# Performance work log

Hardware: AMD Instinct MI355X
Metric: run time of the kernel (lower is better)

## Reference

```python
import jax, jax.numpy as jnp
from jax import lax
import numpy as np

HEADS, SAMPLES = 4, 8
B, C, D, H, W = 1, 64, 16, 64, 64
HD = C // HEADS  # head_dim = 16
BN_EPS = 1e-5


def conv3d(x, w, b=None, pad=0):
    out = lax.conv_general_dilated(
        x, w, (1, 1, 1), [(pad, pad)] * 3,
        dimension_numbers=("NCDHW", "OIDHW", "NCDHW"))
    if b is not None:
        out = out + b[None, :, None, None, None]
    return out


def trilinear_sample(vol, grid):
    # vol: [Dv,Hv,Wv,Cc]; grid: [...,3] with torch grid_sample semantics:
    # grid[...,0] -> x (W axis), grid[...,1] -> y (H axis), grid[...,2] -> z (D axis)
    # align_corners=True, padding_mode='border'. Returns [..., Cc].
    Dv, Hv, Wv, _ = vol.shape
    ix = (grid[..., 0] + 1.0) * 0.5 * (Wv - 1)
    iy = (grid[..., 1] + 1.0) * 0.5 * (Hv - 1)
    iz = (grid[..., 2] + 1.0) * 0.5 * (Dv - 1)
    x0 = jnp.floor(ix); y0 = jnp.floor(iy); z0 = jnp.floor(iz)
    wx = (ix - x0)[..., None]; wy = (iy - y0)[..., None]; wz = (iz - z0)[..., None]
    x0i = jnp.clip(x0.astype(jnp.int32), 0, Wv - 1); x1i = jnp.clip(x0i + 1, 0, Wv - 1)
    y0i = jnp.clip(y0.astype(jnp.int32), 0, Hv - 1); y1i = jnp.clip(y0i + 1, 0, Hv - 1)
    z0i = jnp.clip(z0.astype(jnp.int32), 0, Dv - 1); z1i = jnp.clip(z0i + 1, 0, Dv - 1)
    g = lambda z, y, x: vol[z, y, x]
    out = (g(z0i, y0i, x0i) * (1 - wz) * (1 - wy) * (1 - wx)
           + g(z0i, y0i, x1i) * (1 - wz) * (1 - wy) * wx
           + g(z0i, y1i, x0i) * (1 - wz) * wy * (1 - wx)
           + g(z0i, y1i, x1i) * (1 - wz) * wy * wx
           + g(z1i, y0i, x0i) * wz * (1 - wy) * (1 - wx)
           + g(z1i, y0i, x1i) * wz * (1 - wy) * wx
           + g(z1i, y1i, x0i) * wz * wy * (1 - wx)
           + g(z1i, y1i, x1i) * wz * wy * wx)
    return out


def t_deform(feat_prev, feat_curr, p):
    b, c, d, h, w = feat_curr.shape
    kv = conv3d(feat_prev, p["kv_w"], p["kv_b"])          # [B,2C,D,H,W]
    q = conv3d(feat_curr, p["q_w"], p["q_b"])              # [B,C,D,H,W]
    # offset branch: conv3x3 -> GELU(exact) -> conv3x3(no bias) -> tanh
    o = conv3d(feat_curr, p["off1_w"], p["off1_b"], pad=1)
    o = jax.nn.gelu(o, approximate=False)
    o = jnp.tanh(conv3d(o, p["off2_w"], None, pad=1))      # [B,M*S*3,D,H,W]
    off = o.reshape(b, HEADS, SAMPLES, 3, d, h, w).transpose(0, 1, 4, 5, 6, 2, 3)  # [B,M,D,H,W,S,3]
    zz, yy, xx = jnp.meshgrid(jnp.linspace(-1, 1, d), jnp.linspace(-1, 1, h),
                              jnp.linspace(-1, 1, w), indexing="ij")
    base = jnp.stack((zz, yy, xx), axis=-1).astype(feat_curr.dtype)  # [D,H,W,3]
    scale = jnp.array([d, h, w], dtype=feat_curr.dtype)
    grid = base[None, None, :, :, :, None, :] + off / scale
    grid = jnp.clip(grid, -1.0, 1.0)
    grid = grid.transpose(0, 1, 5, 2, 3, 4, 6).reshape(b * HEADS, SAMPLES, d, h, w, 3)
    # channels-last per (batch,head) volume; avoids torch's explicit repeat over samples
    vols = kv.reshape(b, HEADS, 2 * HD, d, h, w).transpose(0, 1, 3, 4, 5, 2)
    vols = vols.reshape(b * HEADS, d, h, w, 2 * HD)
    sampled = jax.vmap(trilinear_sample)(vols, grid)        # [B*M,S,D,H,W,2*HD]
    sampled = sampled.reshape(b, HEADS, SAMPLES, d, h, w, 2 * HD)
    key, value = sampled[..., :HD], sampled[..., HD:]
    qh = q.reshape(b, HEADS, HD, d, h, w) * (HD ** -0.5)
    attn = jnp.einsum("bmcdhw,bmsdhwc->bmsdhw", qh, key)
    attn = jax.nn.softmax(attn, axis=2)
    fused = jnp.einsum("bmsdhw,bmsdhwc->bmcdhw", attn, value).reshape(b, c, d, h, w)
    out = conv3d(fused, p["out_w"], p["out_b"])
    # BatchNorm3d (eval: running stats) + ReLU
    inv = lax.rsqrt(p["bn_var"] + BN_EPS)
    out = (out - p["bn_mean"][None, :, None, None, None]) * (inv * p["bn_gamma"])[None, :, None, None, None] \
          + p["bn_beta"][None, :, None, None, None]
    return jax.nn.relu(out)


def setup_inputs() -> dict:
    key = jax.random.key(0)
    ks = jax.random.split(key, 16)
    r = lambda k, shp, s=0.05: (jax.random.normal(k, shp, dtype=jnp.float32) * s)
    return {
        "mid_feat": jax.random.normal(ks[0], (B, C, D, H, W), dtype=jnp.float32),
        "occ_feat": jax.random.normal(ks[1], (B, C, D, H, W), dtype=jnp.float32),
        "prev_feat": jax.random.normal(ks[2], (B, C, D, H, W), dtype=jnp.float32),
        "off1_w": r(ks[3], (C, C, 3, 3, 3)), "off1_b": r(ks[4], (C,)),
        "off2_w": r(ks[5], (HEADS * SAMPLES * 3, C, 3, 3, 3)),
        "kv_w": r(ks[6], (2 * C, C, 1, 1, 1)), "kv_b": r(ks[7], (2 * C,)),
        "q_w": r(ks[8], (C, C, 1, 1, 1)), "q_b": r(ks[9], (C,)),
        "out_w": r(ks[10], (C, C, 1, 1, 1)), "out_b": r(ks[11], (C,)),
        "bn_gamma": jnp.ones((C,), jnp.float32), "bn_beta": jnp.zeros((C,), jnp.float32),
        "bn_mean": jnp.zeros((C,), jnp.float32), "bn_var": jnp.ones((C,), jnp.float32),
    }


def reference(mid_feat, occ_feat, prev_feat, off1_w, off1_b, off2_w, kv_w, kv_b,
              q_w, q_b, out_w, out_b, bn_gamma, bn_beta, bn_mean, bn_var):
    p = dict(off1_w=off1_w, off1_b=off1_b, off2_w=off2_w, kv_w=kv_w, kv_b=kv_b,
             q_w=q_w, q_b=q_b, out_w=out_w, out_b=out_b, bn_gamma=bn_gamma,
             bn_beta=bn_beta, bn_mean=bn_mean, bn_var=bn_var)
    d1 = t_deform(mid_feat, occ_feat, p)
    d2 = t_deform(mid_feat, prev_feat, p)
    return jnp.concatenate([mid_feat, d1, d2], axis=1)  # [B,3C,D,H,W]
```

## Files before the change

### kernel.cpp

```cpp
#include <hip/hip_runtime.h>
#include <math.h>

#define DD 16
#define HH 64
#define WW 64
#define VV (DD*HH*WW)
#define CC 64
#define NHEADS 4
#define NSAMP 8
#define HDIM 16

typedef unsigned int uint;
typedef unsigned short ushort;
typedef __attribute__((ext_vector_type(8))) short bf16x8;
typedef __attribute__((ext_vector_type(4))) float f32x4;

__device__ __forceinline__ float clampf(float v, float lo, float hi){ return fminf(fmaxf(v, lo), hi); }
__device__ __forceinline__ int imin(int a, int b){ return a < b ? a : b; }

__device__ __forceinline__ ushort f2bf(float f){
  uint u = __float_as_uint(f);
  uint r = (u + 0x7fffu + ((u>>16)&1u)) >> 16;
  return (ushort)r;
}
__device__ __forceinline__ uint packbf2(float a, float b){
  return (uint)f2bf(a) | ((uint)f2bf(b) << 16);
}
__device__ __forceinline__ float bflo(uint u){ return __uint_as_float(u << 16); }
__device__ __forceinline__ float bfhi(uint u){ return __uint_as_float(u & 0xffff0000u); }
__device__ __forceinline__ float bf2f(ushort u){ return __uint_as_float((uint)u << 16); }

__device__ __forceinline__ float fast_tanh(float x){
  float e = __expf(2.f*x);
  return 1.f - 2.f/(e + 1.f);
}

__global__ __launch_bounds__(256) void pack_in(const float* __restrict__ a,
                                               const float* __restrict__ b,
                                               uint* __restrict__ o){
  int idx = blockIdx.x*256 + threadIdx.x;
  int v4 = (idx & (VV/4 - 1)) * 4;
  int rest = idx >> 14;
  int cp = rest & 31;
  int call = rest >> 5;
  const float* x = call ? b : a;
  float4 f0 = *reinterpret_cast<const float4*>(x + (size_t)(2*cp)*VV + v4);
  float4 f1 = *reinterpret_cast<const float4*>(x + (size_t)(2*cp+1)*VV + v4);
  uint4 pk;
  pk.x = packbf2(f0.x, f1.x);
  pk.y = packbf2(f0.y, f1.y);
  pk.z = packbf2(f0.z, f1.z);
  pk.w = packbf2(f0.w, f1.w);
  *reinterpret_cast<uint4*>(o + (size_t)(call*32+cp)*VV + v4) = pk;
}

__global__ __launch_bounds__(256) void zpair(const uint* __restrict__ vin,
                                             uint* __restrict__ vout){
  int idx = blockIdx.x*256 + threadIdx.x;
  int j = idx & 15;
  int rest = idx >> 4;
  int z = rest & 15;
  uint uz  = vin[idx];
  uint uz1 = vin[(z < 15) ? idx + 16 : idx];
  uint lo = __builtin_amdgcn_perm(uz1, uz, 0x05040100u);
  uint hi = __builtin_amdgcn_perm(uz1, uz, 0x07060302u);
  uint2 pk; pk.x = lo; pk.y = hi;
  *reinterpret_cast<uint2*>(vout + ((size_t)rest << 5) + 2*j) = pk;
}

__global__ void repack_wmfma(const float* __restrict__ w, uint* __restrict__ o, int MG){
  int U = blockIdx.x*256 + threadIdx.x;
  int total = 54*MG*256;
  if (U >= total) return;
  int j2 = U & 3;
  int m  = (U>>2) & 15;
  int q  = (U>>6) & 3;
  int rest = U >> 8;
  int g = rest % MG;
  int s = rest / MG;
  int tap = s >> 1, h = s & 1;
  int co = g*16 + m;
  int ci = h*32 + q*8 + j2*2;
  int base = co*1728 + ci*27 + tap;
  o[U] = packbf2(w[base], w[base + 27]);
}
__global__ void repack_w1mfma(const float* __restrict__ w, uint* __restrict__ o, int MT){
  int U = blockIdx.x*256 + threadIdx.x;
  int total = 2*MT*256;
  if (U >= total) return;
  int j2 = U & 3;
  int lane = (U>>2) & 63;
  int frag = U >> 8;
  int mt = frag % MT;
  int ks = frag / MT;
  int q = lane >> 4, m = lane & 15;
  int co = mt*16 + m;
  int ci = ks*32 + q*8 + j2*2;
  o[U] = packbf2(w[co*CC + ci], w[co*CC + ci + 1]);
}

template<int CO, int EPI>
__global__ __launch_bounds__(256) void conv1_mfma(
    const void* __restrict__ xa, const void* __restrict__ xb,
    const uint* __restrict__ wA, const float* __restrict__ bias,
    void* __restrict__ outp)
{
  constexpr int MT = CO/16;
  constexpr int MW = MT/4;
  __shared__ ushort xt[64*72];
  int tid = threadIdx.x;
  int lane = tid & 63;
  int g = __builtin_amdgcn_readfirstlane(tid >> 6);
  int q = lane >> 4, n = lane & 15;
  int call = blockIdx.x >> 10;
  int v0 = (blockIdx.x & 1023) * 64;
  if constexpr (EPI == 0){
    const float* x = call ? (const float*)xb : (const float*)xa;
    for (int it = tid; it < 64*32; it += 256){
      int vox = it & 63; int cp = it >> 6;
      float a = x[(size_t)(2*cp)*VV + v0 + vox];
      float b = x[(size_t)(2*cp+1)*VV + v0 + vox];
      *reinterpret_cast<uint*>(&xt[vox*72 + 2*cp]) = packbf2(a,b);
    }
  } else {
    const uint* xp = (const uint*)xa + (size_t)call*32*VV;
    for (int it = tid; it < 64*32; it += 256){
      int vox = it & 63; int cp = it >> 6;
      *reinterpret_cast<uint*>(&xt[vox*72 + 2*cp]) = xp[(size_t)cp*VV + v0 + vox];
    }
  }
  __syncthreads();
  f32x4 acc[MW][4];
  #pragma unroll
  for (int mw=0;mw<MW;mw++)
    #pragma unroll
    for (int nt=0;nt<4;nt++){ acc[mw][nt].x=0.f; acc[mw][nt].y=0.f; acc[mw][nt].z=0.f; acc[mw][nt].w=0.f; }
  const char* ldsb = reinterpret_cast<const char*>(xt);
  const char* wac  = reinterpret_cast<const char*>(wA);
  #pragma unroll
  for (int ks=0; ks<2; ks++){
    bf16x8 bfr[4];
    #pragma unroll
    for (int nt=0; nt<4; nt++)
      bfr[nt] = *reinterpret_cast<const bf16x8*>(ldsb + ((nt*16+n)*144 + q*16 + ks*64));
    #pragma unroll
    for (int mw=0; mw<MW; mw++){
      int mt = g*MW + mw;
      bf16x8 af = *reinterpret_cast<const bf16x8*>(wac + (size_t)((ks*MT + mt)*64 + lane)*16);
      #pragma unroll
      for (int nt=0; nt<4; nt++)
        acc[mw][nt] = __builtin_amdgcn_mfma_f32_16x16x32_bf16(af, bfr[nt], acc[mw][nt], 0, 0, 0);
    }
  }
  if constexpr (EPI == 0){
    #pragma unroll
    for (int mw=0; mw<MW; mw++){
      int mt = g*MW + mw;
      int cob = mt*16 + q*4;
      #pragma unroll
      for (int nt=0; nt<4; nt++){
        int v = v0 + nt*16 + n;
        float r0 = acc[mw][nt].x + bias[cob+0];
        float r1 = acc[mw][nt].y + bias[cob+1];
        float r2 = acc[mw][nt].z + bias[cob+2];
        float r3 = acc[mw][nt].w + bias[cob+3];
        int z = v >> 12, y = (v >> 6) & 63, xx = v & 63;
        int head = cob >> 5;
        uint* vols = (uint*)outp;
        uint2 pk; pk.x = packbf2(r0,r1); pk.y = packbf2(r2,r3);
        *reinterpret_cast<uint2*>(vols + ((size_t)head*VV + (size_t)(y*WW+xx)*DD + z)*16 + ((cob&31)>>1)) = pk;
      }
    }
  } else {
    __syncthreads();
    ushort* xr = xt;
    int cob = g*16 + q*4;
    #pragma unroll
    for (int nt=0; nt<4; nt++){
      int vox = nt*16 + n;
      uint2 pk;
      pk.x = packbf2((acc[0][nt].x + bias[cob+0])*0.25f, (acc[0][nt].y + bias[cob+1])*0.25f);
      pk.y = packbf2((acc[0][nt].z + bias[cob+2])*0.25f, (acc[0][nt].w + bias[cob+3])*0.25f);
      *reinterpret_cast<uint2*>(&xr[vox*64 + cob]) = pk;
    }
    __syncthreads();
    char* ob = (char*)((ushort*)outp + (size_t)call*CC*VV) + (size_t)v0*128;
    const char* lb = reinterpret_cast<const char*>(xr);
    #pragma unroll
    for (int k=0; k<2; k++){
      int idx = tid + k*256;
      *reinterpret_cast<uint4*>(ob + idx*16) = *reinterpret_cast<const uint4*>(lb + idx*16);
    }
  }
}

template<int CO, int OUTPK>
__global__ __launch_bounds__(256) void conv3_mfma(
    const uint* __restrict__ xpk,
    const uint* __restrict__ wA, const float* __restrict__ bias,
    void* __restrict__ outp)
{
  constexpr int MG = CO/16;
  constexpr int MROW = CO/32;
  __shared__ ushort xh[300*40];
  int tid = threadIdx.x;
  int lane = tid & 63;
  int w = __builtin_amdgcn_readfirstlane(tid >> 6);
  int q = lane >> 4, n = lane & 15;
  int bid = blockIdx.x;
  int xcd = bid & 7, islot = bid >> 3;
  int call = islot >> 7;
  int z = xcd*2 + ((islot >> 6) & 1);
  int rem = islot & 63;
  int by = (rem >> 3) << 3, bx = (rem & 7) << 3;

  const uint* xinp = xpk + (size_t)call*32*VV;

  int mbase = (w & 1) * MROW;
  int np = w >> 1;
  int lo[2];
  #pragma unroll
  for (int nt=0;nt<2;nt++){
    int vox = (np*2+nt)*16 + n;
    lo[nt] = ((vox>>3)*10 + (vox&7))*80 + q*16;
  }
  f32x4 acc[MROW][2];
  #pragma unroll
  for (int mr=0;mr<MROW;mr++)
    #pragma unroll
    for (int nt=0;nt<2;nt++){ acc[mr][nt].x=0.f; acc[mr][nt].y=0.f; acc[mr][nt].z=0.f; acc[mr][nt].w=0.f; }

  const char* ldsb = reinterpret_cast<const char*>(xh);
  const char* wac  = reinterpret_cast<const char*>(wA);

  uint pa[10], pb[10]; int lofs[10];
  auto load_half = [&](int h){
    #pragma unroll
    for (int k=0;k<10;k++){
      int it = tid + k*256;
      if (it < 2400){
        int cg = it/300; int pos = it - cg*300;
        int dz = pos/100; int rr = pos - dz*100; int dy = rr/10; int dxx = rr - dy*10;
        int gz = z + dz - 1, gy = by + dy - 1, gx = bx + dxx - 1;
        lofs[k] = pos*40 + cg*4;
        uint a = 0u, b = 0u;
        if (gz>=0 && gz<DD && gy>=0 && gy<HH && gx>=0 && gx<WW){
          size_t gv = (size_t)((gz*HH+gy)*WW + gx);
          int cp0 = h*16 + cg*2;
          a = xinp[(size_t)cp0*VV + gv];
          b = xinp[(size_t)(cp0+1)*VV + gv];
        }
        pa[k] = a; pb[k] = b;
      }
    }
  };
  auto write_half = [&](){
    #pragma unroll
    for (int k=0;k<10;k++){
      int it = tid + k*256;
      if (it < 2400){
        uint2 pk; pk.x = pa[k]; pk.y = pb[k];
        *reinterpret_cast<uint2*>(&xh[lofs[k]]) = pk;
      }
    }
  };
  auto compute_half = [&](int h){
    #pragma unroll 3
    for (int tap=0; tap<27; tap++){
      int dz = tap/9; int r9 = tap - dz*9; int dy = r9/3; int dxx = r9 - dy*3;
      int stepOff = (dz*100 + dy*10 + dxx)*80;
      int s = tap*2 + h;
      bf16x8 af[MROW];
      #pragma unroll
      for (int mr=0;mr<MROW;mr++)
        af[mr] = *reinterpret_cast<const bf16x8*>(wac + (size_t)((s*MG + mbase+mr)*64 + lane)*16);
      bf16x8 bf[2];
      #pragma unroll
      for (int nt=0;nt<2;nt++)
        bf[nt] = *reinterpret_cast<const bf16x8*>(ldsb + (lo[nt] + stepOff));
      #pragma unroll
      for (int mr=0;mr<MROW;mr++)
        #pragma unroll
        for (int nt=0;nt<2;nt++)
          acc[mr][nt] = __builtin_amdgcn_mfma_f32_16x16x32_bf16(af[mr], bf[nt], acc[mr][nt], 0, 0, 0);
    }
  };

  load_half(0);
  write_half();
  __syncthreads();
  load_half(1);
  compute_half(0);
  __syncthreads();
  write_half();
  __syncthreads();
  compute_half(1);

  if (OUTPK == 1){
    #pragma unroll
    for (int mr=0; mr<MROW; mr++){
      int cob = (mbase+mr)*16 + q*4;
      #pragma unroll
      for (int nt=0; nt<2; nt++){
        int vox = (np*2+nt)*16 + n;
        int vy = by + (vox>>3), vx = bx + (vox&7);
        size_t gv = (size_t)((z*HH + vy)*WW + vx);
        float r0 = acc[mr][nt].x + bias[cob+0];
        float r1 = acc[mr][nt].y + bias[cob+1];
        float r2 = acc[mr][nt].z + bias[cob+2];
        float r3 = acc[mr][nt].w + bias[cob+3];
        r0 = 0.5f*r0*(1.f + erff(r0*0.70710678118654752f));
        r1 = 0.5f*r1*(1.f + erff(r1*0.70710678118654752f));
        r2 = 0.5f*r2*(1.f + erff(r2*0.70710678118654752f));
        r3 = 0.5f*r3*(1.f + erff(r3*0.70710678118654752f));
        uint* dst = (uint*)outp + (size_t)call*32*VV;
        dst[(size_t)(cob>>1)*VV + gv]     = packbf2(r0,r1);
        dst[(size_t)((cob>>1)+1)*VV + gv] = packbf2(r2,r3);
      }
    }
  } else {
    __syncthreads();
    ushort* xr = xh;
    #pragma unroll
    for (int mr=0; mr<MROW; mr++){
      int cob = (mbase+mr)*16 + q*4;
      #pragma unroll
      for (int nt=0; nt<2; nt++){
        int vox = (np*2+nt)*16 + n;
        uint2 pk;
        pk.x = packbf2(fast_tanh(acc[mr][nt].x), fast_tanh(acc[mr][nt].y));
        pk.y = packbf2(fast_tanh(acc[mr][nt].z), fast_tanh(acc[mr][nt].w));
        *reinterpret_cast<uint2*>(&xr[vox*96 + cob]) = pk;
      }
    }
    __syncthreads();
    ushort* dst = (ushort*)outp + (size_t)call*96*VV;
    const char* lb = reinterpret_cast<const char*>(xr);
    #pragma unroll
    for (int k=0; k<3; k++){
      int idx = tid + k*256;
      int row = idx/96;
      int off = idx - row*96;
      size_t gb = (size_t)((z*HH + by + row)*WW + bx)*192 + (size_t)off*16;
      *reinterpret_cast<uint4*>((char*)dst + gb) = *reinterpret_cast<const uint4*>(lb + idx*16);
    }
  }
}

struct Geom { int x0,x1,y0,y1,z0,z1; float wx,wy,wz; };
__device__ __forceinline__ Geom make_geom(float zb, float yb, float xb,
                                          float o0, float o1, float o2){
  float g0 = clampf(zb + o0*(1.f/16.f), -1.f, 1.f);
  float g1 = clampf(yb + o1*(1.f/64.f), -1.f, 1.f);
  float g2 = clampf(xb + o2*(1.f/64.f), -1.f, 1.f);
  float ix = (g0+1.f)*0.5f*63.f;
  float iy = (g1+1.f)*0.5f*63.f;
  float iz = (g2+1.f)*0.5f*15.f;
  float fx=floorf(ix), fy=floorf(iy), fz=floorf(iz);
  Geom g;
  g.wx = ix-fx; g.wy = iy-fy; g.wz = iz-fz;
  g.x0 = (int)fx; g.x1 = imin(g.x0+1, WW-1);
  g.y0 = (int)fy; g.y1 = imin(g.y0+1, HH-1);
  g.z0 = (int)fz; g.z1 = imin(g.z0+1, DD-1);
  return g;
}

__global__ __launch_bounds__(256) void sample_attn_kernel(
    const ushort* __restrict__ qbuf, const ushort* __restrict__ offbuf,
    const uint* __restrict__ vols, const uint* __restrict__ woA,
    const float* __restrict__ outb, const float* __restrict__ bng,
    const float* __restrict__ bnb, const float* __restrict__ bnm,
    const float* __restrict__ bnv, float* __restrict__ dout)
{
  __shared__ ushort fsb[16*72];
  int t = threadIdx.x;
  int lane = t & 63;
  int m = __builtin_amdgcn_readfirstlane(t >> 6);
  int slot = lane >> 2;
  int r = lane & 3;
  int bid = blockIdx.x;
  int xcd = bid & 7, islot = bid >> 3;
  int call = islot >> 9;
  int z = xcd*2 + ((islot >> 8) & 1);
  int rem = islot & 255;
  int y = rem >> 2;
  int x0 = (rem & 3) << 4;
  int x = x0 + slot;
  int vbase = (z*HH + y)*WW + x0;
  int v = vbase + slot;

  const ushort* qb = qbuf   + (size_t)call*CC*VV;
  const ushort* ob = offbuf + (size_t)call*96*VV;

  uint4 qu = *reinterpret_cast<const uint4*>(qb + (size_t)v*64 + m*16 + (r&1)*8);
  float qf[8];
  qf[0]=bflo(qu.x); qf[1]=bfhi(qu.x); qf[2]=bflo(qu.y); qf[3]=bfhi(qu.y);
  qf[4]=bflo(qu.z); qf[5]=bfhi(qu.z); qf[6]=bflo(qu.w); qf[7]=bfhi(qu.w);

  uint ou[12];
  {
    const uint4* op4 = reinterpret_cast<const uint4*>(ob + (size_t)v*96 + m*24);
    uint4 a = op4[0], b4 = op4[1], c4 = op4[2];
    ou[0]=a.x;  ou[1]=a.y;  ou[2]=a.z;  ou[3]=a.w;
    ou[4]=b4.x; ou[5]=b4.y; ou[6]=b4.z; ou[7]=b4.w;
    ou[8]=c4.x; ou[9]=c4.y; ou[10]=c4.z; ou[11]=c4.w;
  }

  float zbf = -1.f + (float)z*(2.f/15.f);
  float ybf = -1.f + (float)y*(2.f/63.f);
  float xbf = -1.f + (float)x*(2.f/63.f);

  const char* volb = reinterpret_cast<const char*>(vols) + (size_t)m*VV*128;
  float roleK = (r < 2) ? 1.f : 0.f;
  float lrun = 0.f;
  float fused[8];
  #pragma unroll
  for (int c=0;c<8;c++) fused[c]=0.f;

  #pragma unroll
  for (int s=0;s<NSAMP;s++){
    int i0 = 3*s, i1 = 3*s+1, i2 = 3*s+2;
    float o0 = (i0&1) ? bfhi(ou[i0>>1]) : bflo(ou[i0>>1]);
    float o1 = (i1&1) ? bfhi(ou[i1>>1]) : bflo(ou[i1>>1]);
    float o2 = (i2&1) ? bfhi(ou[i2>>1]) : bflo(ou[i2>>1]);
    Geom g = make_geom(zbf,ybf,xbf,o0,o1,o2);
    const char* pz = volb + (g.z0*128 + r*32);
    float wx1 = g.wx, wx0 = 1.f-g.wx;
    float wy1 = g.wy, wy0 = 1.f-g.wy;
    float wz1 = g.wz, wz0 = 1.f-g.wz;
    float acc[8];
    #pragma unroll
    for (int c=0;c<8;c++) acc[c]=0.f;
    #pragma unroll
    for (int ky=0;ky<2;ky++)
    #pragma unroll
    for (int kx=0;kx<2;kx++){
      int cy = ky? g.y1:g.y0, cx = kx? g.x1:g.x0;
      float wyx = (ky? wy1:wy0)*(kx? wx1:wx0);
      float a0 = wyx*wz0, a1 = wyx*wz1;
      uint wzp;
      asm("v_cvt_pk_bf16_f32 %0, %1, %2" : "=v"(wzp) : "v"(a0), "v"(a1));
      const char* p = pz + (((cy<<6) + cx) << 11);
      uint4 u0 = *reinterpret_cast<const uint4*>(p);
      uint4 u1 = *reinterpret_cast<const uint4*>(p + 16);
      asm("v_dot2_f32_bf16 %0, %1, %2, %0" : "+v"(acc[0]) : "v"(u0.x), "v"(wzp));
      asm("v_dot2_f32_bf16 %0, %1, %2, %0" : "+v"(acc[1]) : "v"(u0.y), "v"(wzp));
      asm("v_dot2_f32_bf16 %0, %1, %2, %0" : "+v"(acc[2]) : "v"(u0.z), "v"(wzp));
      asm("v_dot2_f32_bf16 %0, %1, %2, %0" : "+v"(acc[3]) : "v"(u0.w), "v"(wzp));
      asm("v_dot2_f32_bf16 %0, %1, %2, %0" : "+v"(acc[4]) : "v"(u1.x), "v"(wzp));
      asm("v_dot2_f32_bf16 %0, %1, %2, %0" : "+v"(acc[5]) : "v"(u1.y), "v"(wzp));
      asm("v_dot2_f32_bf16 %0, %1, %2, %0" : "+v"(acc[6]) : "v"(u1.z), "v"(wzp));
      asm("v_dot2_f32_bf16 %0, %1, %2, %0" : "+v"(acc[7]) : "v"(u1.w), "v"(wzp));
    }
    float h = qf[0]*acc[0]+qf[1]*acc[1]+qf[2]*acc[2]+qf[3]*acc[3]
            + qf[4]*acc[4]+qf[5]*acc[5]+qf[6]*acc[6]+qf[7]*acc[7];
    h *= roleK;
    h += __shfl_xor(h, 1);
    h += __shfl_xor(h, 2);
    float e = __expf(h);
    lrun += e;
    #pragma unroll
    for (int c=0;c<8;c++) fused[c] += e*acc[c];
  }
  float isum = 1.f/lrun;
  if (r >= 2){
    uint4 pk;
    pk.x = packbf2(fused[0]*isum, fused[1]*isum);
    pk.y = packbf2(fused[2]*isum, fused[3]*isum);
    pk.z = packbf2(fused[4]*isum, fused[5]*isum);
    pk.w = packbf2(fused[6]*isum, fused[7]*isum);
    *reinterpret_cast<uint4*>(&fsb[slot*72 + m*16 + (r&1)*8]) = pk;
  }
  __syncthreads();

  int qq = lane >> 4, n = lane & 15;
  f32x4 acco;
  acco.x=0.f; acco.y=0.f; acco.z=0.f; acco.w=0.f;
  const char* ldsb = reinterpret_cast<const char*>(fsb);
  const char* wac  = reinterpret_cast<const char*>(woA);
  #pragma unroll
  for (int ks=0; ks<2; ks++){
    bf16x8 af = *reinterpret_cast<const bf16x8*>(wac + (size_t)((ks*4 + m)*64 + lane)*16);
    bf16x8 bfv = *reinterpret_cast<const bf16x8*>(ldsb + (n*144 + qq*16 + ks*64));
    acco = __builtin_amdgcn_mfma_f32_16x16x32_bf16(af, bfv, acco, 0, 0, 0);
  }
  int choff = 64 + call*64;
  #pragma unroll
  for (int rr=0; rr<4; rr++){
    int co = m*16 + qq*4 + rr;
    float inv = rsqrtf(bnv[co] + 1e-5f) * bng[co];
    float val = (acco[rr] + outb[co] - bnm[co]) * inv + bnb[co];
    val = fmaxf(val, 0.f);
    dout[(size_t)(choff+co)*VV + vbase + n] = val;
  }
}

extern "C" void kernel_launch(void* const* d_in, const int* in_sizes, int n_in,
                              void* d_out, int out_size, void* d_ws, size_t ws_size,
                              hipStream_t stream){
  (void)in_sizes; (void)n_in; (void)out_size; (void)ws_size;
  const float* mid  = (const float*)d_in[0];
  const float* occ  = (const float*)d_in[1];
  const float* prev = (const float*)d_in[2];
  const float* off1w= (const float*)d_in[3];
  const float* off1b= (const float*)d_in[4];
  const float* off2w= (const float*)d_in[5];
  const float* kvw  = (const float*)d_in[6];
  const float* kvb  = (const float*)d_in[7];
  const float* qw   = (const float*)d_in[8];
  const float* qb   = (const float*)d_in[9];
  const float* outw = (const float*)d_in[10];
  const float* outb = (const float*)d_in[11];
  const float* bng  = (const float*)d_in[12];
  const float* bnb  = (const float*)d_in[13];
  const float* bnm  = (const float*)d_in[14];
  const float* bnv  = (const float*)d_in[15];
  float* out = (float*)d_out;

  uint*   vols  = (uint*)d_ws;
  ushort* qbuf  = (ushort*)(vols + (size_t)4*VV*16);
  uint*   o1pk  = (uint*)(qbuf + (size_t)2*CC*VV);
  ushort* offb  = (ushort*)(o1pk + (size_t)2*32*VV);
  uint*   wA1   = (uint*)(offb + (size_t)2*96*VV);
  uint*   wA2   = wA1 + 55296;
  uint*   wo    = wA2 + 82944;
  uint*   wkv   = wo  + 2048;
  uint*   wq    = wkv + 4096;
  uint*   o0pk  = wq  + 2048;
  uint*   vols2 = o0pk + (size_t)2*32*VV;

  pack_in<<<4096, 256, 0, stream>>>(occ, prev, o0pk);
  repack_wmfma<<<(55296+255)/256, 256, 0, stream>>>(off1w, wA1, 4);
  repack_wmfma<<<(82944+255)/256, 256, 0, stream>>>(off2w, wA2, 6);
  repack_w1mfma<<<8, 256, 0, stream>>>(outw, wo, 4);
  repack_w1mfma<<<16, 256, 0, stream>>>(kvw, wkv, 8);
  repack_w1mfma<<<8, 256, 0, stream>>>(qw, wq, 4);
  conv1_mfma<128,0><<<1024, 256, 0, stream>>>(mid, mid, wkv, kvb, (void*)vols);
  zpair<<<16384, 256, 0, stream>>>(vols, vols2);
  hipMemcpyAsync(out, mid, (size_t)CC*VV*sizeof(float), hipMemcpyDeviceToDevice, stream);
  conv1_mfma<64,1><<<2048, 256, 0, stream>>>(o0pk, nullptr, wq, qb, (void*)qbuf);
  conv3_mfma<64,1><<<2048, 256, 0, stream>>>(o0pk, wA1, off1b, (void*)o1pk);
  conv3_mfma<96,0><<<2048, 256, 0, stream>>>(o1pk, wA2, off1b, (void*)offb);
  sample_attn_kernel<<<8192, 256, 0, stream>>>(qbuf, offb, vols2, wo,
      outb, bng, bnb, bnm, bnv, out);
}
```

Baseline: 368.7 us.

## Drop zpair volume pass and tile conv3 over two z-slices per block

Removes the zpair kernel, which interleaved z and z+1 voxels into a second volume buffer. The sampling kernel now loads the z0 and z1 rows separately from the original volume and pairs them in registers with perm before the bf16 dot2 ops. The 3x3x3 conv kernels now compute two z slices per block with a 4-deep halo tile, halving the block count and reusing the shared-memory halo across both slices. This saves a full volume read/write pass and reduces halo reloads, at the cost of more LDS, more registers, two loads per corner, and extra perm instructions in the sampler.

```diff
diff --git a/kernel.cpp b/kernel.cpp
--- a/kernel.cpp
+++ b/kernel.cpp
@@ -52,20 +52,6 @@
   pk.z = packbf2(f0.z, f1.z);
   pk.w = packbf2(f0.w, f1.w);
   *reinterpret_cast<uint4*>(o + (size_t)(call*32+cp)*VV + v4) = pk;
-}
-
-__global__ __launch_bounds__(256) void zpair(const uint* __restrict__ vin,
-                                             uint* __restrict__ vout){
-  int idx = blockIdx.x*256 + threadIdx.x;
-  int j = idx & 15;
-  int rest = idx >> 4;
-  int z = rest & 15;
-  uint uz  = vin[idx];
-  uint uz1 = vin[(z < 15) ? idx + 16 : idx];
-  uint lo = __builtin_amdgcn_perm(uz1, uz, 0x05040100u);
-  uint hi = __builtin_amdgcn_perm(uz1, uz, 0x07060302u);
-  uint2 pk; pk.x = lo; pk.y = hi;
-  *reinterpret_cast<uint2*>(vout + ((size_t)rest << 5) + 2*j) = pk;
 }
 
 __global__ void repack_wmfma(const float* __restrict__ w, uint* __restrict__ o, int MG){
@@ -202,47 +188,46 @@
 {
   constexpr int MG = CO/16;
   constexpr int MROW = CO/32;
-  __shared__ ushort xh[300*40];
+  __shared__ ushort xh[400*40];
   int tid = threadIdx.x;
   int lane = tid & 63;
   int w = __builtin_amdgcn_readfirstlane(tid >> 6);
   int q = lane >> 4, n = lane & 15;
   int bid = blockIdx.x;
   int xcd = bid & 7, islot = bid >> 3;
-  int call = islot >> 7;
-  int z = xcd*2 + ((islot >> 6) & 1);
+  int call = islot >> 6;
+  int z0 = xcd*2;
   int rem = islot & 63;
   int by = (rem >> 3) << 3, bx = (rem & 7) << 3;
 
   const uint* xinp = xpk + (size_t)call*32*VV;
 
   int mbase = (w & 1) * MROW;
-  int np = w >> 1;
-  int lo[2];
-  #pragma unroll
-  for (int nt=0;nt<2;nt++){
-    int vox = (np*2+nt)*16 + n;
-    lo[nt] = ((vox>>3)*10 + (vox&7))*80 + q*16;
-  }
-  f32x4 acc[MROW][2];
+  int nh = w >> 1;
+  int lo[4];
+  #pragma unroll
+  for (int nt=0;nt<4;nt++){
+    int vl = nt*16 + n;
+    lo[nt] = ((nh*100 + (vl>>3)*10 + (vl&7)))*80 + q*16;
+  }
+  f32x4 acc[MROW][4];
   #pragma unroll
   for (int mr=0;mr<MROW;mr++)
     #pragma unroll
-    for (int nt=0;nt<2;nt++){ acc[mr][nt].x=0.f; acc[mr][nt].y=0.f; acc[mr][nt].z=0.f; acc[mr][nt].w=0.f; }
+    for (int nt=0;nt<4;nt++){ acc[mr][nt].x=0.f; acc[mr][nt].y=0.f; acc[mr][nt].z=0.f; acc[mr][nt].w=0.f; }
 
   const char* ldsb = reinterpret_cast<const char*>(xh);
   const char* wac  = reinterpret_cast<const char*>(wA);
 
-  uint pa[10], pb[10]; int lofs[10];
+  uint pa[13], pb[13];
   auto load_half = [&](int h){
     #pragma unroll
-    for (int k=0;k<10;k++){
+    for (int k=0;k<13;k++){
       int it = tid + k*256;
-      if (it < 2400){
-        int cg = it/300; int pos = it - cg*300;
+      if (it < 3200){
+        int cg = it/400; int pos = it - cg*400;
         int dz = pos/100; int rr = pos - dz*100; int dy = rr/10; int dxx = rr - dy*10;
-        int gz = z + dz - 1, gy = by + dy - 1, gx = bx + dxx - 1;
-        lofs[k] = pos*40 + cg*4;
+        int gz = z0 + dz - 1, gy = by + dy - 1, gx = bx + dxx - 1;
         uint a = 0u, b = 0u;
         if (gz>=0 && gz<DD && gy>=0 && gy<HH && gx>=0 && gx<WW){
           size_t gv = (size_t)((gz*HH+gy)*WW + gx);
@@ -256,11 +241,12 @@
   };
   auto write_half = [&](){
     #pragma unroll
-    for (int k=0;k<10;k++){
+    for (int k=0;k<13;k++){
       int it = tid + k*256;
-      if (it < 2400){
+      if (it < 3200){
+        int cg = it/400; int pos = it - cg*400;
         uint2 pk; pk.x = pa[k]; pk.y = pb[k];
-        *reinterpret_cast<uint2*>(&xh[lofs[k]]) = pk;
+        *reinterpret_cast<uint2*>(&xh[pos*40 + cg*4]) = pk;
       }
     }
   };
@@ -274,14 +260,14 @@
       #pragma unroll
       for (int mr=0;mr<MROW;mr++)
         af[mr] = *reinterpret_cast<const bf16x8*>(wac + (size_t)((s*MG + mbase+mr)*64 + lane)*16);
-      bf16x8 bf[2];
-      #pragma unroll
-      for (int nt=0;nt<2;nt++)
+      bf16x8 bf[4];
+      #pragma unroll
+      for (int nt=0;nt<4;nt++)
         bf[nt] = *reinterpret_cast<const bf16x8*>(ldsb + (lo[nt] + stepOff));
       #pragma unroll
       for (int mr=0;mr<MROW;mr++)
         #pragma unroll
-        for (int nt=0;nt<2;nt++)
+        for (int nt=0;nt<4;nt++)
           acc[mr][nt] = __builtin_amdgcn_mfma_f32_16x16x32_bf16(af[mr], bf[nt], acc[mr][nt], 0, 0, 0);
     }
   };
@@ -301,10 +287,10 @@
     for (int mr=0; mr<MROW; mr++){
       int cob = (mbase+mr)*16 + q*4;
       #pragma unroll
-      for (int nt=0; nt<2; nt++){
-        int vox = (np*2+nt)*16 + n;
-        int vy = by + (vox>>3), vx = bx + (vox&7);
-        size_t gv = (size_t)((z*HH + vy)*WW + vx);
+      for (int nt=0; nt<4; nt++){
+        int vl = nt*16 + n;
+        int vy = by + (vl>>3), vx = bx + (vl&7);
+        size_t gv = (size_t)(((z0+nh)*HH + vy)*WW + vx);
         float r0 = acc[mr][nt].x + bias[cob+0];
         float r1 = acc[mr][nt].y + bias[cob+1];
         float r2 = acc[mr][nt].z + bias[cob+2];
@@ -325,23 +311,24 @@
     for (int mr=0; mr<MROW; mr++){
       int cob = (mbase+mr)*16 + q*4;
       #pragma unroll
-      for (int nt=0; nt<2; nt++){
-        int vox = (np*2+nt)*16 + n;
+      for (int nt=0; nt<4; nt++){
+        int row = nh*64 + nt*16 + n;
         uint2 pk;
         pk.x = packbf2(fast_tanh(acc[mr][nt].x), fast_tanh(acc[mr][nt].y));
         pk.y = packbf2(fast_tanh(acc[mr][nt].z), fast_tanh(acc[mr][nt].w));
-        *reinterpret_cast<uint2*>(&xr[vox*96 + cob]) = pk;
+        *reinterpret_cast<uint2*>(&xr[row*96 + cob]) = pk;
       }
     }
     __syncthreads();
     ushort* dst = (ushort*)outp + (size_t)call*96*VV;
     const char* lb = reinterpret_cast<const char*>(xr);
     #pragma unroll
-    for (int k=0; k<3; k++){
+    for (int k=0; k<6; k++){
       int idx = tid + k*256;
-      int row = idx/96;
-      int off = idx - row*96;
-      size_t gb = (size_t)((z*HH + by + row)*WW + bx)*192 + (size_t)off*16;
+      int chunk = idx/96;
+      int off = idx - chunk*96;
+      int zi = chunk>>3, y8 = chunk&7;
+      size_t gb = (size_t)(((z0+zi)*HH + by + y8)*WW + bx)*192 + (size_t)off*16;
       *reinterpret_cast<uint4*>((char*)dst + gb) = *reinterpret_cast<const uint4*>(lb + idx*16);
     }
   }
@@ -410,7 +397,7 @@
   float ybf = -1.f + (float)y*(2.f/63.f);
   float xbf = -1.f + (float)x*(2.f/63.f);
 
-  const char* volb = reinterpret_cast<const char*>(vols) + (size_t)m*VV*128;
+  const char* volb = reinterpret_cast<const char*>(vols) + (size_t)m*VV*64;
   float roleK = (r < 2) ? 1.f : 0.f;
   float lrun = 0.f;
   float fused[8];
@@ -424,7 +411,8 @@
     float o1 = (i1&1) ? bfhi(ou[i1>>1]) : bflo(ou[i1>>1]);
     float o2 = (i2&1) ? bfhi(ou[i2>>1]) : bflo(ou[i2>>1]);
     Geom g = make_geom(zbf,ybf,xbf,o0,o1,o2);
-    const char* pz = volb + (g.z0*128 + r*32);
+    int tz0 = g.z0*64 + r*16;
+    int tz1 = g.z1*64 + r*16;
     float wx1 = g.wx, wx0 = 1.f-g.wx;
     float wy1 = g.wy, wy0 = 1.f-g.wy;
     float wz1 = g.wz, wz0 = 1.f-g.wz;
@@ -440,17 +428,27 @@
       float a0 = wyx*wz0, a1 = wyx*wz1;
       uint wzp;
       asm("v_cvt_pk_bf16_f32 %0, %1, %2" : "=v"(wzp) : "v"(a0), "v"(a1));
-      const char* p = pz + (((cy<<6) + cx) << 11);
-      uint4 u0 = *reinterpret_cast<const uint4*>(p);
-      uint4 u1 = *reinterpret_cast<const uint4*>(p + 16);
-      asm("v_dot2_f32_bf16 %0, %1, %2, %0" : "+v"(acc[0]) : "v"(u0.x), "v"(wzp));
-      asm("v_dot2_f32_bf16 %0, %1, %2, %0" : "+v"(acc[1]) : "v"(u0.y), "v"(wzp));
-      asm("v_dot2_f32_bf16 %0, %1, %2, %0" : "+v"(acc[2]) : "v"(u0.z), "v"(wzp));
-      asm("v_dot2_f32_bf16 %0, %1, %2, %0" : "+v"(acc[3]) : "v"(u0.w), "v"(wzp));
-      asm("v_dot2_f32_bf16 %0, %1, %2, %0" : "+v"(acc[4]) : "v"(u1.x), "v"(wzp));
-      asm("v_dot2_f32_bf16 %0, %1, %2, %0" : "+v"(acc[5]) : "v"(u1.y), "v"(wzp));
-      asm("v_dot2_f32_bf16 %0, %1, %2, %0" : "+v"(acc[6]) : "v"(u1.z), "v"(wzp));
-      asm("v_dot2_f32_bf16 %0, %1, %2, %0" : "+v"(acc[7]) : "v"(u1.w), "v"(wzp));
+      int tb = ((cy<<6) + cx) << 10;
+      const char* p = volb + tb;
+      uint4 u0 = *reinterpret_cast<const uint4*>(p + tz0);
+      uint4 u1 = *reinterpret_cast<const uint4*>(p + tz1);
+      uint plo, phi;
+      plo = __builtin_amdgcn_perm(u1.x, u0.x, 0x05040100u);
+      phi = __builtin_amdgcn_perm(u1.x, u0.x, 0x07060302u);
+      asm("v_dot2_f32_bf16 %0, %1, %2, %0" : "+v"(acc[0]) : "v"(plo), "v"(wzp));
+      asm("v_dot2_f32_bf16 %0, %1, %2, %0" : "+v"(acc[1]) : "v"(phi), "v"(wzp));
+      plo = __builtin_amdgcn_perm(u1.y, u0.y, 0x05040100u);
+      phi = __builtin_amdgcn_perm(u1.y, u0.y, 0x07060302u);
+      asm("v_dot2_f32_bf16 %0, %1, %2, %0" : "+v"(acc[2]) : "v"(plo), "v"(wzp));
+      asm("v_dot2_f32_bf16 %0, %1, %2, %0" : "+v"(acc[3]) : "v"(phi), "v"(wzp));
+      plo = __builtin_amdgcn_perm(u1.z, u0.z, 0x05040100u);
+      phi = __builtin_amdgcn_perm(u1.z, u0.z, 0x07060302u);
+      asm("v_dot2_f32_bf16 %0, %1, %2, %0" : "+v"(acc[4]) : "v"(plo), "v"(wzp));
+      asm("v_dot2_f32_bf16 %0, %1, %2, %0" : "+v"(acc[5]) : "v"(phi), "v"(wzp));
+      plo = __builtin_amdgcn_perm(u1.w, u0.w, 0x05040100u);
+      phi = __builtin_amdgcn_perm(u1.w, u0.w, 0x07060302u);
+      asm("v_dot2_f32_bf16 %0, %1, %2, %0" : "+v"(acc[6]) : "v"(plo), "v"(wzp));
+      asm("v_dot2_f32_bf16 %0, %1, %2, %0" : "+v"(acc[7]) : "v"(phi), "v"(wzp));
     }
     float h = qf[0]*acc[0]+qf[1]*acc[1]+qf[2]*acc[2]+qf[3]*acc[3]
             + qf[4]*acc[4]+qf[5]*acc[5]+qf[6]*acc[6]+qf[7]*acc[7];
@@ -527,7 +525,6 @@
   uint*   wkv   = wo  + 2048;
   uint*   wq    = wkv + 4096;
   uint*   o0pk  = wq  + 2048;
-  uint*   vols2 = o0pk + (size_t)2*32*VV;
 
   pack_in<<<4096, 256, 0, stream>>>(occ, prev, o0pk);
   repack_wmfma<<<(55296+255)/256, 256, 0, stream>>>(off1w, wA1, 4);
@@ -536,11 +533,10 @@
   repack_w1mfma<<<16, 256, 0, stream>>>(kvw, wkv, 8);
   repack_w1mfma<<<8, 256, 0, stream>>>(qw, wq, 4);
   conv1_mfma<128,0><<<1024, 256, 0, stream>>>(mid, mid, wkv, kvb, (void*)vols);
-  zpair<<<16384, 256, 0, stream>>>(vols, vols2);
   hipMemcpyAsync(out, mid, (size_t)CC*VV*sizeof(float), hipMemcpyDeviceToDevice, stream);
   conv1_mfma<64,1><<<2048, 256, 0, stream>>>(o0pk, nullptr, wq, qb, (void*)qbuf);
-  conv3_mfma<64,1><<<2048, 256, 0, stream>>>(o0pk, wA1, off1b, (void*)o1pk);
-  conv3_mfma<96,0><<<2048, 256, 0, stream>>>(o1pk, wA2, off1b, (void*)offb);
-  sample_attn_kernel<<<8192, 256, 0, stream>>>(qbuf, offb, vols2, wo,
+  conv3_mfma<64,1><<<1024, 256, 0, stream>>>(o0pk, wA1, off1b, (void*)o1pk);
+  conv3_mfma<96,0><<<1024, 256, 0, stream>>>(o1pk, wA2, off1b, (void*)offb);
+  sample_attn_kernel<<<8192, 256, 0, stream>>>(qbuf, offb, vols, wo,
       outb, bng, bnb, bnm, bnv, out);
 }
```

Result: faster. 337.7 us (-8.4%).
